# Optimization experiments

Hardware: AMD Instinct MI355X
Metric: run time of the kernel (lower is better)

Reference implementation:

```python
import jax, jax.numpy as jnp
import numpy as np

EMBED = 768
HEADS = 12
DEPTH = 12
PATCH = 16
IMG = 512
TOK = IMG // PATCH          # 32 tokens per side
WIN = 14                    # SAM window size
GLOBAL = (2, 5, 8, 11)      # global-attention block indices (vit_b)
HD = EMBED // HEADS         # 64 head dim
MLP = 4 * EMBED
OUT = 256                   # neck out_chans
EPS = 1e-6


def setup_inputs() -> dict:
    key = jax.random.key(0)
    ks = jax.random.split(key, 32)
    f32 = jnp.float32
    def n(k, shape, s=0.02):
        return jax.random.normal(k, shape, dtype=f32) * s
    return {
        'x': jax.random.normal(ks[0], (1, 3, IMG, IMG), dtype=f32),
        'patch_w': n(ks[1], (EMBED, 3, PATCH, PATCH)),
        'patch_b': jnp.zeros((EMBED,), f32),
        'pos_embed': n(ks[2], (1, TOK, TOK, EMBED)),
        'qkv_w': n(ks[3], (DEPTH, 3 * EMBED, EMBED)),
        'qkv_b': jnp.zeros((DEPTH, 3 * EMBED), f32),
        'proj_w': n(ks[4], (DEPTH, EMBED, EMBED)),
        'proj_b': jnp.zeros((DEPTH, EMBED), f32),
        'norm1_w': jnp.ones((DEPTH, EMBED), f32),
        'norm1_b': jnp.zeros((DEPTH, EMBED), f32),
        'norm2_w': jnp.ones((DEPTH, EMBED), f32),
        'norm2_b': jnp.zeros((DEPTH, EMBED), f32),
        'mlp_w1': n(ks[5], (DEPTH, MLP, EMBED)),
        'mlp_b1': jnp.zeros((DEPTH, MLP), f32),
        'mlp_w2': n(ks[6], (DEPTH, EMBED, MLP)),
        'mlp_b2': jnp.zeros((DEPTH, EMBED), f32),
        'rel_h_win': n(ks[7], (DEPTH, 2 * WIN - 1, HD)),
        'rel_w_win': n(ks[8], (DEPTH, 2 * WIN - 1, HD)),
        'rel_h_glob': n(ks[9], (DEPTH, 2 * TOK - 1, HD)),
        'rel_w_glob': n(ks[10], (DEPTH, 2 * TOK - 1, HD)),
        'neck_w1': n(ks[11], (OUT, EMBED)),
        'neck_ln1_w': jnp.ones((OUT,), f32),
        'neck_ln1_b': jnp.zeros((OUT,), f32),
        'neck_w2': n(ks[12], (OUT, OUT, 3, 3)),
        'neck_ln2_w': jnp.ones((OUT,), f32),
        'neck_ln2_b': jnp.zeros((OUT,), f32),
    }


def _ln(x, w, b):
    u = x.mean(-1, keepdims=True)
    s = ((x - u) ** 2).mean(-1, keepdims=True)
    return (x - u) / jnp.sqrt(s + EPS) * w + b


def _ln2d(y, w, b):
    # LayerNorm over channel dim of NCHW
    u = y.mean(1, keepdims=True)
    s = ((y - u) ** 2).mean(1, keepdims=True)
    return (y - u) / jnp.sqrt(s + EPS) * w[None, :, None, None] + b[None, :, None, None]


def _window_partition(x, ws):
    B, H, W, C = x.shape
    ph, pw = (ws - H % ws) % ws, (ws - W % ws) % ws
    x = jnp.pad(x, ((0, 0), (0, ph), (0, pw), (0, 0)))
    Hp, Wp = H + ph, W + pw
    x = x.reshape(B, Hp // ws, ws, Wp // ws, ws, C).transpose(0, 1, 3, 2, 4, 5)
    return x.reshape(-1, ws, ws, C), (Hp, Wp)


def _window_unpartition(win, ws, pad_hw, hw):
    Hp, Wp = pad_hw
    H, W = hw
    B = win.shape[0] // ((Hp // ws) * (Wp // ws))
    x = win.reshape(B, Hp // ws, Wp // ws, ws, ws, -1).transpose(0, 1, 3, 2, 4, 5)
    return x.reshape(B, Hp, Wp, -1)[:, :H, :W]


def _attention(x, qkv_w, qkv_b, proj_w, proj_b, rel_h, rel_w):
    # x: (B, H, W, C); decomposed rel-pos added to attn scores (SAM style)
    B, H, W, C = x.shape
    N = H * W
    qkv = x.reshape(B, N, C) @ qkv_w.T + qkv_b                     # (B,N,3C)
    qkv = qkv.reshape(B, N, 3, HEADS, HD).transpose(2, 0, 3, 1, 4)
    qkv = qkv.reshape(3, B * HEADS, N, HD)
    q, k, v = qkv[0], qkv[1], qkv[2]
    attn = (q * (HD ** -0.5)) @ k.transpose(0, 2, 1)               # (B*nh,N,N)
    idx_h = jnp.arange(H)[:, None] - jnp.arange(H)[None, :] + (H - 1)
    idx_w = jnp.arange(W)[:, None] - jnp.arange(W)[None, :] + (W - 1)
    Rh = rel_h[idx_h]                                              # (H,H,hd)
    Rw = rel_w[idx_w]                                              # (W,W,hd)
    rq = q.reshape(-1, H, W, HD)
    bias_h = jnp.einsum('bhwc,hkc->bhwk', rq, Rh)
    bias_w = jnp.einsum('bhwc,wkc->bhwk', rq, Rw)
    attn = attn.reshape(-1, H, W, H, W) + bias_h[:, :, :, :, None] + bias_w[:, :, :, None, :]
    attn = jax.nn.softmax(attn.reshape(-1, N, N), axis=-1)
    out = (attn @ v).reshape(B, HEADS, H, W, HD).transpose(0, 2, 3, 1, 4).reshape(B, H, W, C)
    return out @ proj_w.T + proj_b


def reference(x, patch_w, patch_b, pos_embed, qkv_w, qkv_b, proj_w, proj_b,
              norm1_w, norm1_b, norm2_w, norm2_b, mlp_w1, mlp_b1, mlp_w2, mlp_b2,
              rel_h_win, rel_w_win, rel_h_glob, rel_w_glob,
              neck_w1, neck_ln1_w, neck_ln1_b, neck_w2, neck_ln2_w, neck_ln2_b):
    # patch embed: 16x16 stride-16 conv, then NHWC
    h = jax.lax.conv_general_dilated(x, patch_w, (PATCH, PATCH), 'VALID',
                                     dimension_numbers=('NCHW', 'OIHW', 'NCHW'))
    h = h.transpose(0, 2, 3, 1) + patch_b
    h = h + pos_embed
    for i in range(DEPTH):
        glob = i in GLOBAL
        rh = rel_h_glob[i] if glob else rel_h_win[i]
        rw = rel_w_glob[i] if glob else rel_w_win[i]
        shortcut = h
        t = _ln(h, norm1_w[i], norm1_b[i])
        if not glob:
            t, pad_hw = _window_partition(t, WIN)
        t = _attention(t, qkv_w[i], qkv_b[i], proj_w[i], proj_b[i], rh, rw)
        if not glob:
            t = _window_unpartition(t, WIN, pad_hw, (TOK, TOK))
        h = shortcut + t
        t = _ln(h, norm2_w[i], norm2_b[i])
        t = jax.nn.gelu(t @ mlp_w1[i].T + mlp_b1[i], approximate=False) @ mlp_w2[i].T + mlp_b2[i]
        h = h + t
    # neck: 1x1 conv -> LN2d -> 3x3 conv -> LN2d (convs bias-free)
    y = h.transpose(0, 3, 1, 2)
    y = jnp.einsum('bchw,oc->bohw', y, neck_w1)
    y = _ln2d(y, neck_ln1_w, neck_ln1_b)
    y = jax.lax.conv_general_dilated(y, neck_w2, (1, 1), 'SAME',
                                     dimension_numbers=('NCHW', 'OIHW', 'NCHW'))
    y = _ln2d(y, neck_ln2_w, neck_ln2_b)
    return y
```

## Files before the change

kernel.cpp:

```cpp
#include <hip/hip_runtime.h>
#include <math.h>

#define EMBED   768
#define HEADS   12
#define DEPTH   12
#define TOKS    32
#define NTOK    1024
#define WINSZ   14
#define NWIN    9
#define WTOK    1764
#define WN      196
#define MLPDIM  3072
#define OUTC    256
#define LNEPS   1e-6f

typedef __attribute__((ext_vector_type(8))) short short8;
typedef __attribute__((ext_vector_type(4))) float float4v;

__device__ __forceinline__ unsigned short f2bf(float f) {
    unsigned u = __float_as_uint(f);
    unsigned r = (u + 0x7fffu + ((u >> 16) & 1u)) >> 16;
    return (unsigned short)r;
}
__device__ __forceinline__ float bf2f(unsigned short s) {
    return __uint_as_float((unsigned)s << 16);
}
__device__ __forceinline__ unsigned cvtpk(float a, float b) {
    unsigned r;
    asm("v_cvt_pk_bf16_f32 %0, %1, %2" : "=v"(r) : "v"(a), "v"(b));
    return r;
}
__device__ __forceinline__ short8 pk8(float4 a, float4 b) {
    union { unsigned u[4]; short8 s; } t;
    t.u[0] = cvtpk(a.x, a.y); t.u[1] = cvtpk(a.z, a.w);
    t.u[2] = cvtpk(b.x, b.y); t.u[3] = cvtpk(b.z, b.w);
    return t.s;
}
__device__ __forceinline__ int winidx(int p) {
    int gy = p >> 5, gx = p & 31;
    return ((gy / WINSZ) * 3 + gx / WINSZ) * WN + (gy % WINSZ) * WINSZ + (gx % WINSZ);
}


__global__ __launch_bounds__(256) void convw_all(
        const float* __restrict__ q,  const float* __restrict__ pr,
        const float* __restrict__ m1, const float* __restrict__ m2,
        const float* __restrict__ pw, const float* __restrict__ n1,
        const float* __restrict__ n2,
        unsigned short* __restrict__ oq,  unsigned short* __restrict__ opr,
        unsigned short* __restrict__ om1, unsigned short* __restrict__ om2,
        unsigned short* __restrict__ opw, unsigned short* __restrict__ on1,
        unsigned short* __restrict__ on2) {
    int g = blockIdx.x * 256 + threadIdx.x;
    const float* s; unsigned short* o; int off; int K;
    if (g < 2654208)        { s = q;  o = oq;  off = g;            K = 768;  }
    else if (g < 3538944)   { s = pr; o = opr; off = g - 2654208;  K = 768;  }
    else if (g < 7077888)   { s = m1; o = om1; off = g - 3538944;  K = 768;  }
    else if (g < 10616832)  { s = m2; o = om2; off = g - 7077888;  K = 3072; }
    else if (g < 10690560)  { s = pw; o = opw; off = g - 10616832; K = 768;  }
    else if (g < 10715136)  { s = n1; o = on1; off = g - 10690560; K = 768;  }
    else                    { s = n2; o = on2; off = g - 10715136; K = 2304; }
    int twoK = 2 * K;
    int rb = off / twoK, rem = off - rb * twoK;
    int kc = rem >> 4, rl = rem & 15;
    const float* sp = s + (size_t)(rb * 16 + rl) * K + kc * 8;
    float4 v0 = *(const float4*)sp, v1 = *(const float4*)(sp + 4);
    *(short8*)(o + (size_t)off * 8) = pk8(v0, v1);
}

__global__ __launch_bounds__(256) void convw_one(
        const float* __restrict__ in, unsigned short* __restrict__ out,
        int K, int nchunk) {
    int g = blockIdx.x * 256 + threadIdx.x;
    if (g >= nchunk) return;
    int twoK = 2 * K;
    int rb = g / twoK, rem = g - rb * twoK;
    int kc = rem >> 4, rl = rem & 15;
    const float* sp = in + (size_t)(rb * 16 + rl) * K + kc * 8;
    float4 v0 = *(const float4*)sp, v1 = *(const float4*)(sp + 4);
    *(short8*)(out + (size_t)g * 8) = pk8(v0, v1);
}

__global__ __launch_bounds__(256) void zero_pads(unsigned short* __restrict__ XWw) {
    int t = blockIdx.x;
    int w = t / WN, r = t % WN;
    int gy = (w / 3) * WINSZ + r / WINSZ, gx = (w % 3) * WINSZ + r % WINSZ;
    if (gy < TOKS && gx < TOKS) return;
    unsigned short* dst = XWw + (size_t)(t >> 4) * 12288 + (size_t)(t & 15) * 8;
    for (int c = threadIdx.x; c < EMBED; c += 256)
        dst[(size_t)(c >> 3) * 128 + (c & 7)] = 0;
}

#define LDT(S, KO) do {                                               \
    _Pragma("unroll")                                                 \
    for (int i_ = 0; i_ < 2; i_++) {                                  \
        a_##S[i_][0] = *(const short8*)(ap[i_] + (size_t)(KO) * AKS); \
        a_##S[i_][1] = *(const short8*)(ap[i_] + (size_t)(KO) * AKS + 32 * AKS); } \
    _Pragma("unroll")                                                 \
    for (int j_ = 0; j_ < 2; j_++) {                                  \
        b_##S[j_][0] = *(const short8*)(bp[j_] + (size_t)(KO) * 16);  \
        b_##S[j_][1] = *(const short8*)(bp[j_] + (size_t)(KO) * 16 + 512); } \
} while (0)

#define MFMA_SLOT(S) do {                                       \
    _Pragma("unroll")                                           \
    for (int h_ = 0; h_ < 2; h_++)                              \
        _Pragma("unroll")                                       \
        for (int i_ = 0; i_ < 2; i_++)                          \
            _Pragma("unroll")                                   \
            for (int j_ = 0; j_ < 2; j_++)                      \
                acc[i_][j_] = __builtin_amdgcn_mfma_f32_16x16x32_bf16( \
                    a_##S[i_][h_], b_##S[j_][h_], acc[i_][j_], 0, 0, 0); \
} while (0)

template<int OMODE, int SPLIT, int NT, int AT>
__global__ __launch_bounds__(256) void gemm_rd(
        const unsigned short* __restrict__ A, const unsigned short* __restrict__ B,
        const float* __restrict__ bias, void* __restrict__ Cout,
        int M, int N, int K,
        unsigned short* __restrict__ vout, int VN, int VNP) {
    const int tid = threadIdx.x, lane = tid & 63, wave = tid >> 6;
    const int wm = wave >> 1, wn = wave & 1;
    const int l15 = lane & 15, q4 = lane >> 4;
    const int AKS = AT ? 16 : 1;

    const int gx = gridDim.x, gy = gridDim.y;
    const int nb = gx * gy;
    const int f  = blockIdx.y * gx + blockIdx.x;
    const int qq = nb >> 3, rr = nb & 7;
    const int xcd = f & 7, sl = f >> 3;
    const int wg = (xcd < rr) ? xcd * (qq + 1) + sl
                              : rr * (qq + 1) + (xcd - rr) * qq + sl;
    const int bn = wg / gy;
    const int bm = wg - bn * gy;

    const int m0 = bm * 64 + wm * 32;
    const int n0 = bn * 64 + wn * 32;
    const int kb = blockIdx.z * (NT * 64);
    const int Kc8 = K >> 3;

    const unsigned short* ap[2];
    if (AT) {
#pragma unroll
        for (int i = 0; i < 2; i++) {
            int mb = (m0 + i * 16) >> 4;
            ap[i] = A + ((size_t)mb * Kc8 + (kb >> 3)) * 128 + q4 * 128 + l15 * 8;
        }
    } else {
#pragma unroll
        for (int i = 0; i < 2; i++) {
            int gm = m0 + i * 16 + l15; if (gm >= M) gm = M - 1;
            ap[i] = A + (size_t)gm * K + kb + q4 * 8;
        }
    }
    const unsigned short* bp[2];
#pragma unroll
    for (int j = 0; j < 2; j++) {
        int nb2 = (n0 + j * 16) >> 4;
        bp[j] = B + ((size_t)nb2 * Kc8 + (kb >> 3)) * 128 + q4 * 128 + l15 * 8;
    }

    float4v acc[2][2];
#pragma unroll
    for (int i = 0; i < 2; i++)
#pragma unroll
        for (int j = 0; j < 2; j++) acc[i][j] = (float4v){0.f, 0.f, 0.f, 0.f};

    short8 a_0[2][2], b_0[2][2];
    short8 a_1[2][2], b_1[2][2];
    short8 a_2[2][2], b_2[2][2];

    LDT(0, 0);
    LDT(1, 64);
#pragma unroll
    for (int k = 0; k + 3 < NT; k += 3) {
        LDT(2, (k + 2) * 64); MFMA_SLOT(0);
        LDT(0, (k + 3) * 64); MFMA_SLOT(1);
        LDT(1, (k + 4) * 64); MFMA_SLOT(2);
    }
    LDT(2, (NT - 1) * 64);
    MFMA_SLOT(0); MFMA_SLOT(1); MFMA_SLOT(2);

    if (SPLIT > 1) {
        float* P = (float*)Cout + (size_t)blockIdx.z * M * N;
#pragma unroll
        for (int i = 0; i < 2; i++)
#pragma unroll
            for (int r = 0; r < 4; r++) {
                int m = m0 + i * 16 + q4 * 4 + r;
                if (m >= M) continue;
#pragma unroll
                for (int j = 0; j < 2; j++)
                    P[(size_t)m * N + n0 + j * 16 + l15] = acc[i][j][r];
            }
        return;
    }
#pragma unroll
    for (int i = 0; i < 2; i++) {
        int mb = m0 + i * 16 + q4 * 4;
#pragma unroll
        for (int j = 0; j < 2; j++) {
            int n = n0 + j * 16 + l15;
            float bv = bias ? bias[n] : 0.f;
            if (OMODE == 3 && n >= 1536) {
                int nn = n - 1536;
                int head = nn >> 6, dd = nn & 63;
                if (mb + 3 < M) {
                    int win = mb / VN, mt = mb - win * VN;
                    ushort4 o;
                    o.x = f2bf(acc[i][j][0] + bv);
                    o.y = f2bf(acc[i][j][1] + bv);
                    o.z = f2bf(acc[i][j][2] + bv);
                    o.w = f2bf(acc[i][j][3] + bv);
                    *(ushort4*)(vout + (size_t)((win * HEADS + head) * 64 + dd) * VNP + mt) = o;
                } else {
#pragma unroll
                    for (int r = 0; r < 4; r++) {
                        int m = mb + r;
                        if (m >= M) continue;
                        int win = m / VN, mt = m - win * VN;
                        vout[(size_t)((win * HEADS + head) * 64 + dd) * VNP + mt] =
                            f2bf(acc[i][j][r] + bv);
                    }
                }
                continue;
            }
#pragma unroll
            for (int r = 0; r < 4; r++) {
                int m = mb + r;
                if (m >= M) continue;
                float v = acc[i][j][r] + bv;
                if (OMODE == 0) {
                    ((float*)Cout)[(size_t)m * N + n] = v;
                } else if (OMODE == 2) {
                    v = 0.5f * v * (1.f + erff(v * 0.70710678118654752f));
                    ((unsigned short*)Cout)[(size_t)m * N + n] = f2bf(v);
                } else {
                    ((unsigned short*)Cout)[(size_t)m * 2304 + n] = f2bf(v);
                }
            }
        }
    }
}

template<int S>
__global__ __launch_bounds__(256) void fuse_ln(
        const float* __restrict__ part, size_t pstride, int partwin,
        const float* __restrict__ extra, const float* __restrict__ bias,
        float* __restrict__ H, int addH,
        const float* __restrict__ lnw, const float* __restrict__ lnb,
        unsigned short* __restrict__ lnout, int lnmode) {
    const int p = blockIdx.x;
    const int tw = winidx(p);
    const int tp = partwin ? tw : p;
    const int c0 = threadIdx.x;
    float h[3];
    float s1 = 0.f, s2 = 0.f;
#pragma unroll
    for (int j = 0; j < 3; j++) {
        int c = c0 + j * 256;
        float v = 0.f;
        if (S > 0) {
            v = part[(size_t)tp * EMBED + c];
#pragma unroll
            for (int z = 1; z < S; z++) v += part[(size_t)z * pstride + (size_t)tp * EMBED + c];
            v += bias[c];
        }
        if (extra) v += extra[(size_t)p * EMBED + c];
        if (addH)  v += H[(size_t)p * EMBED + c];
        h[j] = v;
        if (S > 0) H[(size_t)p * EMBED + c] = v;
        s1 += v; s2 += v * v;
    }
    for (int off = 32; off; off >>= 1) {
        s1 += __shfl_down(s1, off);
        s2 += __shfl_down(s2, off);
    }
    __shared__ float sh1[4], sh2[4];
    __shared__ float smu, srstd;
    int wv = threadIdx.x >> 6, ln = threadIdx.x & 63;
    if (ln == 0) { sh1[wv] = s1; sh2[wv] = s2; }
    __syncthreads();
    if (threadIdx.x == 0) {
        float t1 = sh1[0] + sh1[1] + sh1[2] + sh1[3];
        float t2 = sh2[0] + sh2[1] + sh2[2] + sh2[3];
        float m = t1 / (float)EMBED;
        smu = m; srstd = rsqrtf(t2 / (float)EMBED - m * m + LNEPS);
    }
    __syncthreads();
    float m = smu, r = srstd;
    int R = (lnmode == 2) ? tw : p;
    unsigned short* dst = lnout + (size_t)(R >> 4) * 12288 + (size_t)(R & 15) * 8;
#pragma unroll
    for (int j = 0; j < 3; j++) {
        int c = c0 + j * 256;
        float v = (lnmode == 3) ? h[j] : (h[j] - m) * r * lnw[c] + lnb[c];
        dst[(size_t)(c >> 3) * 128 + (c & 7)] = f2bf(v);
    }
}

template<int S>
__global__ __launch_bounds__(256) void fuse_ln_neck(
        const float* __restrict__ part, const float* __restrict__ w,
        const float* __restrict__ b, float* __restrict__ out, int M, int mode) {
    const int row = blockIdx.x, c = threadIdx.x;
    float v = part[(size_t)row * OUTC + c];
#pragma unroll
    for (int z = 1; z < S; z++)
        v += part[(size_t)z * M * OUTC + (size_t)row * OUTC + c];
    float s1 = v, s2 = v * v;
    for (int off = 32; off; off >>= 1) {
        s1 += __shfl_down(s1, off);
        s2 += __shfl_down(s2, off);
    }
    __shared__ float sh1[4], sh2[4];
    __shared__ float smu, srs;
    int wv = threadIdx.x >> 6, ln = threadIdx.x & 63;
    if (ln == 0) { sh1[wv] = s1; sh2[wv] = s2; }
    __syncthreads();
    if (threadIdx.x == 0) {
        float t1 = sh1[0] + sh1[1] + sh1[2] + sh1[3];
        float t2 = sh2[0] + sh2[1] + sh2[2] + sh2[3];
        float m = t1 / (float)OUTC;
        smu = m; srs = rsqrtf(t2 / (float)OUTC - m * m + LNEPS);
    }
    __syncthreads();
    float res = (v - smu) * srs * w[c] + b[c];
    if (mode == 0) out[(size_t)row * OUTC + c] = res;
    else           out[(size_t)c * M + row] = res;
}

template<int N, int HH, int WW, int VNP>
__global__ __launch_bounds__(256) void attn_mfma(
        const unsigned short* __restrict__ qkv, const unsigned short* __restrict__ vt,
        const float* __restrict__ rel_h, const float* __restrict__ rel_w,
        unsigned short* __restrict__ out) {
    constexpr int NT = (N + 63) / 64;
    constexpr int JH = ((2 * HH - 1 + 15) / 16) * 16;
    constexpr int JW = ((2 * WW - 1 + 15) / 16) * 16;
    __shared__ unsigned short Pw[4][16 * 72];
    __shared__ float Dh[4][16][JH];
    __shared__ float Dw[4][16][JW];
    const int tid = threadIdx.x, lane = tid & 63, w = tid >> 6;
    const int l15 = lane & 15, q4 = lane >> 4;
    const int bh = blockIdx.y, winI = bh / HEADS, head = bh % HEADS;
    const int base = winI * N;
    const int q0 = blockIdx.x * 64;

    short8 aq0, aq1;
    {
        int qr = q0 + w * 16 + l15; if (qr >= N) qr = N - 1;
        const unsigned short* qp = qkv + (size_t)(base + qr) * 2304 + head * 64;
        aq0 = *(const short8*)(qp + q4 * 8);
        aq1 = *(const short8*)(qp + 32 + q4 * 8);
    }

#pragma unroll
    for (int s = 0; s < JH / 16; s++) {
        int j = s * 16 + l15; if (j > 2 * HH - 2) j = 2 * HH - 2;
        const float* rp = rel_h + (size_t)j * 64 + q4 * 8;
        float4 r0 = *(const float4*)rp;
        float4 r1 = *(const float4*)(rp + 4);
        float4 r2 = *(const float4*)(rp + 32);
        float4 r3 = *(const float4*)(rp + 36);
        short8 b0 = pk8(r0, r1), b1 = pk8(r2, r3);
        float4v df = (float4v){0.f, 0.f, 0.f, 0.f};
        df = __builtin_amdgcn_mfma_f32_16x16x32_bf16(aq0, b0, df, 0, 0, 0);
        df = __builtin_amdgcn_mfma_f32_16x16x32_bf16(aq1, b1, df, 0, 0, 0);
#pragma unroll
        for (int r = 0; r < 4; r++) Dh[w][q4 * 4 + r][s * 16 + l15] = df[r];
    }
#pragma unroll
    for (int s = 0; s < JW / 16; s++) {
        int j = s * 16 + l15; if (j > 2 * WW - 2) j = 2 * WW - 2;
        const float* rp = rel_w + (size_t)j * 64 + q4 * 8;
        float4 r0 = *(const float4*)rp;
        float4 r1 = *(const float4*)(rp + 4);
        float4 r2 = *(const float4*)(rp + 32);
        float4 r3 = *(const float4*)(rp + 36);
        short8 b0 = pk8(r0, r1), b1 = pk8(r2, r3);
        float4v df = (float4v){0.f, 0.f, 0.f, 0.f};
        df = __builtin_amdgcn_mfma_f32_16x16x32_bf16(aq0, b0, df, 0, 0, 0);
        df = __builtin_amdgcn_mfma_f32_16x16x32_bf16(aq1, b1, df, 0, 0, 0);
#pragma unroll
        for (int r = 0; r < 4; r++) Dw[w][q4 * 4 + r][s * 16 + l15] = df[r];
    }

    int qhv[4], qwv[4];
#pragma unroll
    for (int r = 0; r < 4; r++) {
        int qg = q0 + w * 16 + q4 * 4 + r;
        qhv[r] = qg / WW;
        qwv[r] = qg - qhv[r] * WW;
    }

    float m_r[4], l_r[4];
    float4v acc_o[4];
#pragma unroll
    for (int r = 0; r < 4; r++) { m_r[r] = -1e30f; l_r[r] = 0.f; }
#pragma unroll
    for (int s = 0; s < 4; s++) acc_o[s] = (float4v){0.f, 0.f, 0.f, 0.f};

    const unsigned short* vbase = vt + (size_t)bh * 64 * VNP;
    const unsigned short* kqbase = qkv + (size_t)base * 2304 + 768 + head * 64;

    short8 kc[8];
#pragma unroll
    for (int s = 0; s < 4; s++) {
        int kr = s * 16 + l15; if (kr >= N) kr = N - 1;
        const unsigned short* kp = kqbase + (size_t)kr * 2304;
        kc[2 * s]     = *(const short8*)(kp + q4 * 8);
        kc[2 * s + 1] = *(const short8*)(kp + 32 + q4 * 8);
    }

    for (int kt = 0; kt < NT; kt++) {
        short8 vv[8];
        {
            const unsigned short* vb = vbase + kt * 64;
#pragma unroll
            for (int s2 = 0; s2 < 4; s2++) {
                const unsigned short* vr = vb + (size_t)(s2 * 16 + l15) * VNP;
                vv[2 * s2]     = *(const short8*)(vr + q4 * 8);
                vv[2 * s2 + 1] = *(const short8*)(vr + 32 + q4 * 8);
            }
        }
        short8 kn[8];
        {
            int ktn = (kt + 1 < NT) ? kt + 1 : kt;
#pragma unroll
            for (int s = 0; s < 4; s++) {
                int kr = ktn * 64 + s * 16 + l15; if (kr >= N) kr = N - 1;
                const unsigned short* kp = kqbase + (size_t)kr * 2304;
                kn[2 * s]     = *(const short8*)(kp + q4 * 8);
                kn[2 * s + 1] = *(const short8*)(kp + 32 + q4 * 8);
            }
        }
        float sv[4][4];
#pragma unroll
        for (int s = 0; s < 4; s++) {
            float4v sf = (float4v){0.f, 0.f, 0.f, 0.f};
            sf = __builtin_amdgcn_mfma_f32_16x16x32_bf16(aq0, kc[2 * s], sf, 0, 0, 0);
            sf = __builtin_amdgcn_mfma_f32_16x16x32_bf16(aq1, kc[2 * s + 1], sf, 0, 0, 0);
            int col = kt * 64 + s * 16 + l15;
            if (col < N) {
                int kh = col / WW, kw = col - kh * WW;
#pragma unroll
                for (int r = 0; r < 4; r++)
                    sv[s][r] = sf[r] * 0.125f
                             + Dh[w][q4 * 4 + r][qhv[r] - kh + HH - 1]
                             + Dw[w][q4 * 4 + r][qwv[r] - kw + WW - 1];
            } else {
#pragma unroll
                for (int r = 0; r < 4; r++) sv[s][r] = -1e30f;
            }
        }
        float p[4][4];
#pragma unroll
        for (int r = 0; r < 4; r++) {
            float t = fmaxf(fmaxf(sv[0][r], sv[1][r]), fmaxf(sv[2][r], sv[3][r]));
#pragma unroll
            for (int off = 1; off < 16; off <<= 1) t = fmaxf(t, __shfl_xor(t, off));
            float mn = fmaxf(m_r[r], t);
            float alpha = __expf(m_r[r] - mn);
            m_r[r] = mn;
            float ps = 0.f;
#pragma unroll
            for (int s = 0; s < 4; s++) { p[s][r] = __expf(sv[s][r] - mn); ps += p[s][r]; }
#pragma unroll
            for (int off = 1; off < 16; off <<= 1) ps += __shfl_xor(ps, off);
            l_r[r] = l_r[r] * alpha + ps;
#pragma unroll
            for (int s = 0; s < 4; s++) acc_o[s][r] *= alpha;
        }
#pragma unroll
        for (int s = 0; s < 4; s++)
#pragma unroll
            for (int r = 0; r < 4; r++)
                Pw[w][(q4 * 4 + r) * 72 + s * 16 + l15] = f2bf(p[s][r]);
        short8 af0 = *(const short8*)(&Pw[w][l15 * 72 + q4 * 8]);
        short8 af1 = *(const short8*)(&Pw[w][l15 * 72 + 32 + q4 * 8]);
#pragma unroll
        for (int s2 = 0; s2 < 4; s2++) {
            acc_o[s2] = __builtin_amdgcn_mfma_f32_16x16x32_bf16(af0, vv[2 * s2], acc_o[s2], 0, 0, 0);
            acc_o[s2] = __builtin_amdgcn_mfma_f32_16x16x32_bf16(af1, vv[2 * s2 + 1], acc_o[s2], 0, 0, 0);
        }
#pragma unroll
        for (int i = 0; i < 8; i++) kc[i] = kn[i];
    }
#pragma unroll
    for (int r = 0; r < 4; r++) {
        int qg = q0 + w * 16 + q4 * 4 + r;
        if (qg >= N) continue;
        float inv = 1.f / l_r[r];
#pragma unroll
        for (int s2 = 0; s2 < 4; s2++)
            out[(size_t)(base + qg) * EMBED + head * 64 + s2 * 16 + l15] =
                f2bf(acc_o[s2][r] * inv);
    }
}

__global__ void im2col_patch(const float* __restrict__ x, unsigned short* __restrict__ A, int n) {
    int i = blockIdx.x * blockDim.x + threadIdx.x;
    if (i >= n) return;
    int t = i / EMBED, kidx = i % EMBED;
    int c = kidx >> 8, r = kidx & 255;
    int ph = r >> 4, pw = r & 15;
    int ty = t >> 5, tx = t & 31;
    A[i] = f2bf(x[(size_t)c * 512 * 512 + (size_t)(ty * 16 + ph) * 512 + (tx * 16 + pw)]);
}

__global__ void im2col3(const float* __restrict__ in, unsigned short* __restrict__ out, int n) {
    int i = blockIdx.x * blockDim.x + threadIdx.x;
    if (i >= n) return;
    int p = i / 2304, k = i % 2304;
    int c = k / 9, r9 = k % 9;
    int ky = r9 / 3, kx = r9 % 3;
    int py = p >> 5, px = p & 31;
    int ny = py + ky - 1, nx = px + kx - 1;
    float v = (ny >= 0 && ny < TOKS && nx >= 0 && nx < TOKS)
                ? in[(size_t)(ny * TOKS + nx) * OUTC + c] : 0.f;
    out[i] = f2bf(v);
}

extern "C" void kernel_launch(void* const* d_in, const int* in_sizes, int n_in,
                              void* d_out, int out_size, void* d_ws, size_t ws_size,
                              hipStream_t stream) {
    const float* x        = (const float*)d_in[0];
    const float* patch_w  = (const float*)d_in[1];
    const float* patch_b  = (const float*)d_in[2];
    const float* pos      = (const float*)d_in[3];
    const float* qkv_w    = (const float*)d_in[4];
    const float* qkv_b    = (const float*)d_in[5];
    const float* proj_w   = (const float*)d_in[6];
    const float* proj_b   = (const float*)d_in[7];
    const float* n1w      = (const float*)d_in[8];
    const float* n1b      = (const float*)d_in[9];
    const float* n2w      = (const float*)d_in[10];
    const float* n2b      = (const float*)d_in[11];
    const float* mlp_w1   = (const float*)d_in[12];
    const float* mlp_b1   = (const float*)d_in[13];
    const float* mlp_w2   = (const float*)d_in[14];
    const float* mlp_b2   = (const float*)d_in[15];
    const float* rhw      = (const float*)d_in[16];
    const float* rww      = (const float*)d_in[17];
    const float* rhg      = (const float*)d_in[18];
    const float* rwg      = (const float*)d_in[19];
    const float* neck_w1  = (const float*)d_in[20];
    const float* nl1w     = (const float*)d_in[21];
    const float* nl1b     = (const float*)d_in[22];
    const float* neck_w2  = (const float*)d_in[23];
    const float* nl2w     = (const float*)d_in[24];
    const float* nl2b     = (const float*)d_in[25];

    const size_t SZ_QKVW = (size_t)2304 * 768;
    const size_t SZ_PROJ = (size_t)768 * 768;
    const size_t SZ_MLP1 = (size_t)3072 * 768;
    const size_t SZ_MLP2 = (size_t)768 * 3072;

    char* p = (char*)d_ws;
    float* H    = (float*)p;            p += (size_t)NTOK * EMBED * 4;
    unsigned short* QKVb = (unsigned short*)p; p += (size_t)WTOK * 2304 * 2;
    unsigned short* Vt   = (unsigned short*)p; p += (size_t)NWIN * HEADS * 64 * 208 * 2 + 4096;
    float* LNF  = (float*)p;            p += (size_t)NTOK * OUTC * 4;
    unsigned short* XWw = (unsigned short*)p;  p += (size_t)112 * 12288 * 2;
    unsigned short* XWs = (unsigned short*)p;  p += (size_t)64 * 12288 * 2;
    unsigned short* AOb = (unsigned short*)p;  p += (size_t)WTOK * EMBED * 2;
    float* SPK  = (float*)p;            p += (size_t)16 * 1024 * 1024;
    unsigned short* PWb  = (unsigned short*)p; p += SZ_PROJ * 2;
    unsigned short* NW1b = (unsigned short*)p; p += (size_t)OUTC * 768 * 2;
    unsigned short* NW2b = (unsigned short*)p; p += (size_t)OUTC * 2304 * 2;
    unsigned short* MIDB  = QKVb;
    unsigned short* CONVA = QKVb;

    unsigned short* WQa = (unsigned short*)p;
    size_t needAll = (size_t)(p - (char*)d_ws) +
                     (SZ_QKVW + SZ_PROJ + SZ_MLP1 + SZ_MLP2) * 2 * DEPTH;
    bool pre = ws_size >= needAll;
    unsigned short *WPa, *W1a, *W2a;
    size_t sQ, sP, s1, s2;
    if (pre) {
        WPa = WQa + SZ_QKVW * DEPTH;
        W1a = WPa + SZ_PROJ * DEPTH;
        W2a = W1a + SZ_MLP1 * DEPTH;
        sQ = SZ_QKVW; sP = SZ_PROJ; s1 = SZ_MLP1; s2 = SZ_MLP2;
    } else {
        WPa = WQa + SZ_QKVW;
        W1a = WPa + SZ_PROJ;
        W2a = W1a + SZ_MLP1;
        sQ = sP = s1 = s2 = 0;
    }

    const int NE = NTOK * EMBED;

    zero_pads<<<WTOK, 256, 0, stream>>>(XWw);
    if (pre) {
        convw_all<<<42144, 256, 0, stream>>>(
            qkv_w, proj_w, mlp_w1, mlp_w2, patch_w, neck_w1, neck_w2,
            WQa, WPa, W1a, W2a, PWb, NW1b, NW2b);
    } else {
        convw_one<<<(73728 + 255) / 256, 256, 0, stream>>>(patch_w, PWb, 768, 73728);
        convw_one<<<(24576 + 255) / 256, 256, 0, stream>>>(neck_w1, NW1b, 768, 24576);
        convw_one<<<(73728 + 255) / 256, 256, 0, stream>>>(neck_w2, NW2b, 2304, 73728);
    }

    im2col_patch<<<(NE + 255) / 256, 256, 0, stream>>>(x, AOb, NE);
    gemm_rd<0, 2, 6, 0><<<dim3(EMBED / 64, NTOK / 64, 2), 256, 0, stream>>>(
        AOb, PWb, nullptr, SPK, NTOK, EMBED, EMBED, nullptr, 0, 0);
    fuse_ln<2><<<NTOK, 256, 0, stream>>>(
        SPK, (size_t)NTOK * EMBED, 0, pos, patch_b, H, 0, n1w, n1b, XWw, 2);

    for (int i = 0; i < DEPTH; i++) {
        bool glob = (i == 2 || i == 5 || i == 8 || i == 11);
        const unsigned short* wq = WQa + sQ * i;
        const unsigned short* wp = WPa + sP * i;
        const unsigned short* w1 = W1a + s1 * i;
        const unsigned short* w2 = W2a + s2 * i;
        if (!pre) {
            convw_one<<<(2212 * 100 + 255) / 256, 256, 0, stream>>>(
                qkv_w + (size_t)i * SZ_QKVW, WQa, 768, 221184);
            convw_one<<<(73728 + 255) / 256, 256, 0, stream>>>(
                proj_w + (size_t)i * SZ_PROJ, WPa, 768, 73728);
            convw_one<<<(294912 + 255) / 256, 256, 0, stream>>>(
                mlp_w1 + (size_t)i * SZ_MLP1, W1a, 768, 294912);
            convw_one<<<(294912 + 255) / 256, 256, 0, stream>>>(
                mlp_w2 + (size_t)i * SZ_MLP2, W2a, 3072, 294912);
        }

        if (!glob) {
            gemm_rd<3, 1, 12, 1><<<dim3(2304 / 64, (WTOK + 63) / 64), 256, 0, stream>>>(
                XWw, wq, qkv_b + i * 2304, QKVb, WTOK, 2304, EMBED, Vt, WN, 208);
            attn_mfma<WN, WINSZ, WINSZ, 208><<<dim3(4, NWIN * HEADS), 256, 0, stream>>>(
                QKVb, Vt, rhw + (size_t)i * 27 * 64, rww + (size_t)i * 27 * 64, AOb);
            gemm_rd<0, 2, 6, 0><<<dim3(EMBED / 64, (WTOK + 63) / 64, 2), 256, 0, stream>>>(
                AOb, wp, nullptr, SPK, WTOK, EMBED, EMBED, nullptr, 0, 0);
            fuse_ln<2><<<NTOK, 256, 0, stream>>>(
                SPK, (size_t)WTOK * EMBED, 1, nullptr, proj_b + i * EMBED, H, 1,
                n2w + i * EMBED, n2b + i * EMBED, XWs, 1);
        } else {
            gemm_rd<3, 1, 12, 1><<<dim3(2304 / 64, NTOK / 64), 256, 0, stream>>>(
                XWs, wq, qkv_b + i * 2304, QKVb, NTOK, 2304, EMBED, Vt, NTOK, NTOK);
            attn_mfma<NTOK, TOKS, TOKS, NTOK><<<dim3(16, HEADS), 256, 0, stream>>>(
                QKVb, Vt, rhg + (size_t)i * 63 * 64, rwg + (size_t)i * 63 * 64, AOb);
            gemm_rd<0, 2, 6, 0><<<dim3(EMBED / 64, NTOK / 64, 2), 256, 0, stream>>>(
                AOb, wp, nullptr, SPK, NTOK, EMBED, EMBED, nullptr, 0, 0);
            fuse_ln<2><<<NTOK, 256, 0, stream>>>(
                SPK, (size_t)NTOK * EMBED, 0, nullptr, proj_b + i * EMBED, H, 1,
                n2w + i * EMBED, n2b + i * EMBED, XWs, 1);
        }
        gemm_rd<2, 1, 12, 1><<<dim3(MLPDIM / 64, NTOK / 64), 256, 0, stream>>>(
            XWs, w1, mlp_b1 + i * MLPDIM, MIDB, NTOK, MLPDIM, EMBED, nullptr, 0, 0);
        gemm_rd<0, 4, 12, 0><<<dim3(EMBED / 64, NTOK / 64, 4), 256, 0, stream>>>(
            MIDB, w2, nullptr, SPK, NTOK, EMBED, MLPDIM, nullptr, 0, 0);
        int nlnmode; const float* nw; const float* nb2; unsigned short* ndst;
        if (i == DEPTH - 1) { nlnmode = 3; nw = n1w; nb2 = n1b; ndst = XWs; }
        else {
            bool nglob = (i + 1 == 2 || i + 1 == 5 || i + 1 == 8 || i + 1 == 11);
            nlnmode = nglob ? 1 : 2;
            nw = n1w + (size_t)(i + 1) * EMBED; nb2 = n1b + (size_t)(i + 1) * EMBED;
            ndst = nglob ? XWs : XWw;
        }
        fuse_ln<4><<<NTOK, 256, 0, stream>>>(
            SPK, (size_t)NTOK * EMBED, 0, nullptr, mlp_b2 + i * EMBED, H, 1,
            nw, nb2, ndst, nlnmode);
    }

    gemm_rd<0, 4, 3, 1><<<dim3(OUTC / 64, NTOK / 64, 4), 256, 0, stream>>>(
        XWs, NW1b, nullptr, SPK, NTOK, OUTC, EMBED, nullptr, 0, 0);
    fuse_ln_neck<4><<<NTOK, 256, 0, stream>>>(SPK, nl1w, nl1b, LNF, NTOK, 0);
    im2col3<<<(NTOK * 2304 + 255) / 256, 256, 0, stream>>>(LNF, CONVA, NTOK * 2304);
    gemm_rd<0, 6, 6, 0><<<dim3(OUTC / 64, NTOK / 64, 6), 256, 0, stream>>>(
        CONVA, NW2b, nullptr, SPK, NTOK, OUTC, 2304, nullptr, 0, 0);
    fuse_ln_neck<6><<<NTOK, 256, 0, stream>>>(SPK, nl2w, nl2b, (float*)d_out, NTOK, 1);
}
```

Measured before the change: 1.763 ms.

## Write GEMM A-operands in tiled MFMA layout and pad window rows

Every producer of a GEMM A operand (patch im2col, attention output, GELU MLP hidden, neck im2col) now writes bf16 data in a 16-row by 8-column tiled layout. This lets the proj, MLP2, patch and neck GEMMs use the tiled-load path (last template flag set to 1). Window-attention rows are padded to a 256-row pitch per window so the proj GEMM M is a multiple of 64. The one-time weight conversion kernel is rewritten to transpose through shared memory for coalesced stores. The changes aim to cut strided A-operand loads, at the cost of extra padded rows in the windowed proj GEMM.

```diff
diff --git a/kernel.cpp b/kernel.cpp
--- a/kernel.cpp
+++ b/kernel.cpp
@@ -10,6 +10,7 @@
 #define NWIN    9
 #define WTOK    1764
 #define WN      196
+#define WPITCH  256
 #define MLPDIM  3072
 #define OUTC    256
 #define LNEPS   1e-6f
@@ -51,21 +52,31 @@
         unsigned short* __restrict__ om1, unsigned short* __restrict__ om2,
         unsigned short* __restrict__ opw, unsigned short* __restrict__ on1,
         unsigned short* __restrict__ on2) {
-    int g = blockIdx.x * 256 + threadIdx.x;
-    const float* s; unsigned short* o; int off; int K;
-    if (g < 2654208)        { s = q;  o = oq;  off = g;            K = 768;  }
-    else if (g < 3538944)   { s = pr; o = opr; off = g - 2654208;  K = 768;  }
-    else if (g < 7077888)   { s = m1; o = om1; off = g - 3538944;  K = 768;  }
-    else if (g < 10616832)  { s = m2; o = om2; off = g - 7077888;  K = 3072; }
-    else if (g < 10690560)  { s = pw; o = opw; off = g - 10616832; K = 768;  }
-    else if (g < 10715136)  { s = n1; o = on1; off = g - 10690560; K = 768;  }
-    else                    { s = n2; o = on2; off = g - 10715136; K = 2304; }
-    int twoK = 2 * K;
-    int rb = off / twoK, rem = off - rb * twoK;
-    int kc = rem >> 4, rl = rem & 15;
-    const float* sp = s + (size_t)(rb * 16 + rl) * K + kc * 8;
-    float4 v0 = *(const float4*)sp, v1 = *(const float4*)(sp + 4);
-    *(short8*)(o + (size_t)off * 8) = pk8(v0, v1);
+    __shared__ unsigned short L[16][136];
+    int g = blockIdx.x;
+    const float* s; unsigned short* o; int blk; int K;
+    if (g < 10368)       { s = q;  o = oq;  blk = g;         K = 768;  }
+    else if (g < 13824)  { s = pr; o = opr; blk = g - 10368; K = 768;  }
+    else if (g < 27648)  { s = m1; o = om1; blk = g - 13824; K = 768;  }
+    else if (g < 41472)  { s = m2; o = om2; blk = g - 27648; K = 3072; }
+    else if (g < 41760)  { s = pw; o = opw; blk = g - 41472; K = 768;  }
+    else if (g < 41856)  { s = n1; o = on1; blk = g - 41760; K = 768;  }
+    else                 { s = n2; o = on2; blk = g - 41856; K = 2304; }
+    int nkb = K >> 7;
+    int rb = blk / nkb, kcb = blk - rb * nkb;
+    int t = threadIdx.x;
+    {
+        int rl = t >> 4, cl = (t & 15) * 8;
+        const float* sp = s + (size_t)(rb * 16 + rl) * K + kcb * 128 + cl;
+        float4 v0 = *(const float4*)sp, v1 = *(const float4*)(sp + 4);
+        *(short8*)&L[rl][cl] = pk8(v0, v1);
+    }
+    __syncthreads();
+    {
+        int kc_l = t >> 4, rw = t & 15;
+        short8 vv = *(const short8*)&L[rw][kc_l * 8];
+        *(short8*)(o + ((size_t)(rb * (K >> 3) + kcb * 16 + kc_l) * 16 + rw) * 8) = vv;
+    }
 }
 
 __global__ __launch_bounds__(256) void convw_one(
@@ -234,7 +245,8 @@
                     ((float*)Cout)[(size_t)m * N + n] = v;
                 } else if (OMODE == 2) {
                     v = 0.5f * v * (1.f + erff(v * 0.70710678118654752f));
-                    ((unsigned short*)Cout)[(size_t)m * N + n] = f2bf(v);
+                    ((unsigned short*)Cout)[((size_t)(m >> 4) * (N >> 3) + (n >> 3)) * 128
+                                            + (m & 15) * 8 + (n & 7)] = f2bf(v);
                 } else {
                     ((unsigned short*)Cout)[(size_t)m * 2304 + n] = f2bf(v);
                 }
@@ -252,7 +264,7 @@
         unsigned short* __restrict__ lnout, int lnmode) {
     const int p = blockIdx.x;
     const int tw = winidx(p);
-    const int tp = partwin ? tw : p;
+    const int tp = partwin ? ((tw / WN) * WPITCH + (tw % WN)) : p;
     const int c0 = threadIdx.x;
     float h[3];
     float s1 = 0.f, s2 = 0.f;
@@ -330,7 +342,7 @@
     else           out[(size_t)c * M + row] = res;
 }
 
-template<int N, int HH, int WW, int VNP>
+template<int N, int HH, int WW, int VNP, int ROWP>
 __global__ __launch_bounds__(256) void attn_mfma(
         const unsigned short* __restrict__ qkv, const unsigned short* __restrict__ vt,
         const float* __restrict__ rel_h, const float* __restrict__ rel_w,
@@ -491,11 +503,14 @@
     for (int r = 0; r < 4; r++) {
         int qg = q0 + w * 16 + q4 * 4 + r;
         if (qg >= N) continue;
+        int rowT = winI * ROWP + qg;
         float inv = 1.f / l_r[r];
-#pragma unroll
-        for (int s2 = 0; s2 < 4; s2++)
-            out[(size_t)(base + qg) * EMBED + head * 64 + s2 * 16 + l15] =
-                f2bf(acc_o[s2][r] * inv);
+        unsigned short* dst = out + (size_t)(rowT >> 4) * 12288 + (size_t)(rowT & 15) * 8;
+#pragma unroll
+        for (int s2 = 0; s2 < 4; s2++) {
+            int col = head * 64 + s2 * 16 + l15;
+            dst[(size_t)(col >> 3) * 128 + (col & 7)] = f2bf(acc_o[s2][r] * inv);
+        }
     }
 }
 
@@ -506,7 +521,8 @@
     int c = kidx >> 8, r = kidx & 255;
     int ph = r >> 4, pw = r & 15;
     int ty = t >> 5, tx = t & 31;
-    A[i] = f2bf(x[(size_t)c * 512 * 512 + (size_t)(ty * 16 + ph) * 512 + (tx * 16 + pw)]);
+    float v = x[(size_t)c * 512 * 512 + (size_t)(ty * 16 + ph) * 512 + (tx * 16 + pw)];
+    A[((size_t)(t >> 4) * 96 + (kidx >> 3)) * 128 + (t & 15) * 8 + (kidx & 7)] = f2bf(v);
 }
 
 __global__ void im2col3(const float* __restrict__ in, unsigned short* __restrict__ out, int n) {
@@ -519,7 +535,7 @@
     int ny = py + ky - 1, nx = px + kx - 1;
     float v = (ny >= 0 && ny < TOKS && nx >= 0 && nx < TOKS)
                 ? in[(size_t)(ny * TOKS + nx) * OUTC + c] : 0.f;
-    out[i] = f2bf(v);
+    out[((size_t)(p >> 4) * 288 + (k >> 3)) * 128 + (p & 15) * 8 + (k & 7)] = f2bf(v);
 }
 
 extern "C" void kernel_launch(void* const* d_in, const int* in_sizes, int n_in,
@@ -556,6 +572,7 @@
     const size_t SZ_PROJ = (size_t)768 * 768;
     const size_t SZ_MLP1 = (size_t)3072 * 768;
     const size_t SZ_MLP2 = (size_t)768 * 3072;
+    const int MPAD = NWIN * WPITCH;
 
     char* p = (char*)d_ws;
     float* H    = (float*)p;            p += (size_t)NTOK * EMBED * 4;
@@ -564,7 +581,7 @@
     float* LNF  = (float*)p;            p += (size_t)NTOK * OUTC * 4;
     unsigned short* XWw = (unsigned short*)p;  p += (size_t)112 * 12288 * 2;
     unsigned short* XWs = (unsigned short*)p;  p += (size_t)64 * 12288 * 2;
-    unsigned short* AOb = (unsigned short*)p;  p += (size_t)WTOK * EMBED * 2;
+    unsigned short* AOb = (unsigned short*)p;  p += (size_t)144 * 96 * 128 * 2;
     float* SPK  = (float*)p;            p += (size_t)16 * 1024 * 1024;
     unsigned short* PWb  = (unsigned short*)p; p += SZ_PROJ * 2;
     unsigned short* NW1b = (unsigned short*)p; p += (size_t)OUTC * 768 * 2;
@@ -604,7 +621,7 @@
     }
 
     im2col_patch<<<(NE + 255) / 256, 256, 0, stream>>>(x, AOb, NE);
-    gemm_rd<0, 2, 6, 0><<<dim3(EMBED / 64, NTOK / 64, 2), 256, 0, stream>>>(
+    gemm_rd<0, 2, 6, 1><<<dim3(EMBED / 64, NTOK / 64, 2), 256, 0, stream>>>(
         AOb, PWb, nullptr, SPK, NTOK, EMBED, EMBED, nullptr, 0, 0);
     fuse_ln<2><<<NTOK, 256, 0, stream>>>(
         SPK, (size_t)NTOK * EMBED, 0, pos, patch_b, H, 0, n1w, n1b, XWw, 2);
@@ -616,7 +633,7 @@
         const unsigned short* w1 = W1a + s1 * i;
         const unsigned short* w2 = W2a + s2 * i;
         if (!pre) {
-            convw_one<<<(2212 * 100 + 255) / 256, 256, 0, stream>>>(
+            convw_one<<<(221184 + 255) / 256, 256, 0, stream>>>(
                 qkv_w + (size_t)i * SZ_QKVW, WQa, 768, 221184);
             convw_one<<<(73728 + 255) / 256, 256, 0, stream>>>(
                 proj_w + (size_t)i * SZ_PROJ, WPa, 768, 73728);
@@ -629,19 +646,19 @@
         if (!glob) {
             gemm_rd<3, 1, 12, 1><<<dim3(2304 / 64, (WTOK + 63) / 64), 256, 0, stream>>>(
                 XWw, wq, qkv_b + i * 2304, QKVb, WTOK, 2304, EMBED, Vt, WN, 208);
-            attn_mfma<WN, WINSZ, WINSZ, 208><<<dim3(4, NWIN * HEADS), 256, 0, stream>>>(
+            attn_mfma<WN, WINSZ, WINSZ, 208, WPITCH><<<dim3(4, NWIN * HEADS), 256, 0, stream>>>(
                 QKVb, Vt, rhw + (size_t)i * 27 * 64, rww + (size_t)i * 27 * 64, AOb);
-            gemm_rd<0, 2, 6, 0><<<dim3(EMBED / 64, (WTOK + 63) / 64, 2), 256, 0, stream>>>(
-                AOb, wp, nullptr, SPK, WTOK, EMBED, EMBED, nullptr, 0, 0);
+            gemm_rd<0, 2, 6, 1><<<dim3(EMBED / 64, MPAD / 64, 2), 256, 0, stream>>>(
+                AOb, wp, nullptr, SPK, MPAD, EMBED, EMBED, nullptr, 0, 0);
             fuse_ln<2><<<NTOK, 256, 0, stream>>>(
-                SPK, (size_t)WTOK * EMBED, 1, nullptr, proj_b + i * EMBED, H, 1,
+                SPK, (size_t)MPAD * EMBED, 1, nullptr, proj_b + i * EMBED, H, 1,
                 n2w + i * EMBED, n2b + i * EMBED, XWs, 1);
         } else {
             gemm_rd<3, 1, 12, 1><<<dim3(2304 / 64, NTOK / 64), 256, 0, stream>>>(
                 XWs, wq, qkv_b + i * 2304, QKVb, NTOK, 2304, EMBED, Vt, NTOK, NTOK);
-            attn_mfma<NTOK, TOKS, TOKS, NTOK><<<dim3(16, HEADS), 256, 0, stream>>>(
+            attn_mfma<NTOK, TOKS, TOKS, NTOK, NTOK><<<dim3(16, HEADS), 256, 0, stream>>>(
                 QKVb, Vt, rhg + (size_t)i * 63 * 64, rwg + (size_t)i * 63 * 64, AOb);
-            gemm_rd<0, 2, 6, 0><<<dim3(EMBED / 64, NTOK / 64, 2), 256, 0, stream>>>(
+            gemm_rd<0, 2, 6, 1><<<dim3(EMBED / 64, NTOK / 64, 2), 256, 0, stream>>>(
                 AOb, wp, nullptr, SPK, NTOK, EMBED, EMBED, nullptr, 0, 0);
             fuse_ln<2><<<NTOK, 256, 0, stream>>>(
                 SPK, (size_t)NTOK * EMBED, 0, nullptr, proj_b + i * EMBED, H, 1,
@@ -649,7 +666,7 @@
         }
         gemm_rd<2, 1, 12, 1><<<dim3(MLPDIM / 64, NTOK / 64), 256, 0, stream>>>(
             XWs, w1, mlp_b1 + i * MLPDIM, MIDB, NTOK, MLPDIM, EMBED, nullptr, 0, 0);
-        gemm_rd<0, 4, 12, 0><<<dim3(EMBED / 64, NTOK / 64, 4), 256, 0, stream>>>(
+        gemm_rd<0, 4, 12, 1><<<dim3(EMBED / 64, NTOK / 64, 4), 256, 0, stream>>>(
             MIDB, w2, nullptr, SPK, NTOK, EMBED, MLPDIM, nullptr, 0, 0);
         int nlnmode; const float* nw; const float* nb2; unsigned short* ndst;
         if (i == DEPTH - 1) { nlnmode = 3; nw = n1w; nb2 = n1b; ndst = XWs; }
@@ -668,7 +685,7 @@
         XWs, NW1b, nullptr, SPK, NTOK, OUTC, EMBED, nullptr, 0, 0);
     fuse_ln_neck<4><<<NTOK, 256, 0, stream>>>(SPK, nl1w, nl1b, LNF, NTOK, 0);
     im2col3<<<(NTOK * 2304 + 255) / 256, 256, 0, stream>>>(LNF, CONVA, NTOK * 2304);
-    gemm_rd<0, 6, 6, 0><<<dim3(OUTC / 64, NTOK / 64, 6), 256, 0, stream>>>(
+    gemm_rd<0, 6, 6, 1><<<dim3(OUTC / 64, NTOK / 64, 6), 256, 0, stream>>>(
         CONVA, NW2b, nullptr, SPK, NTOK, OUTC, 2304, nullptr, 0, 0);
     fuse_ln_neck<6><<<NTOK, 256, 0, stream>>>(SPK, nl2w, nl2b, (float*)d_out, NTOK, 1);
 }
```

New measurement: 1.621 ms. 8.0% less time.
